# Kernel optimization log

Measured on AMD Instinct MI355X. Metric: run time of the kernel, lower is better.

The kernel has to match this reference:

```python
import jax, jax.numpy as jnp
import numpy as np

B, S, D, F = 8, 2048, 1024, 3072
EPS = 1e-6


def _rmsnorm(x, w):
    rms = jax.lax.rsqrt(jnp.mean(x * x, axis=-1, keepdims=True) + EPS)
    return x * rms * w


def _scan_causal(x_scan, a):
    # h_t = a_t * h_{t-1} + x_t, over time axis. x_scan, a: [B,S,D]
    def step(h, inp):
        xs, at = inp
        h = at * h + xs
        return h, h
    xs_t = jnp.swapaxes(x_scan, 0, 1)  # [S,B,D]
    a_t = jnp.swapaxes(a, 0, 1)
    h0 = jnp.zeros(x_scan.shape[::2], dtype=x_scan.dtype)  # [B,D]
    _, out = jax.lax.scan(step, h0, (xs_t, a_t))
    return jnp.swapaxes(out, 0, 1)  # [B,S,D]


def setup_inputs() -> dict:
    key = jax.random.key(0)
    ks = jax.random.split(key, 12)
    sd = 1.0 / np.sqrt(D)
    sf = 1.0 / np.sqrt(F)
    return {
        "x": jax.random.normal(ks[0], (B, S, D), dtype=jnp.float32),
        "rms_mix_w": jnp.ones((D,), jnp.float32),
        "rms_ffn_w": jnp.ones((D,), jnp.float32),
        "Wg": jax.random.uniform(ks[1], (D, D), jnp.float32, -sd, sd),
        "bg": jax.random.uniform(ks[2], (D,), jnp.float32, -sd, sd),
        "Wv": jax.random.uniform(ks[3], (D, D), jnp.float32, -sd, sd),
        "bv": jax.random.uniform(ks[4], (D,), jnp.float32, -sd, sd),
        "Wd": jax.random.uniform(ks[5], (D, D), jnp.float32, -sd, sd),
        "bd": jnp.full((D,), 1.0, jnp.float32),  # decay_bias_init = 1.0
        "W_gate": jax.random.uniform(ks[6], (F, D), jnp.float32, -sd, sd),
        "W_up": jax.random.uniform(ks[7], (F, D), jnp.float32, -sd, sd),
        "W_out": jax.random.uniform(ks[8], (D, F), jnp.float32, -sf, sf),
    }


def reference(x, rms_mix_w, rms_ffn_w, Wg, bg, Wv, bv, Wd, bd, W_gate, W_up, W_out):
    # --- MinGRU mixer with pre-RMSNorm and residual ---
    xn = _rmsnorm(x, rms_mix_w)
    g = jnp.einsum("bsd,ed->bse", xn, Wg) + bg
    v = jnp.einsum("bsd,ed->bse", xn, Wv) + bv
    d = jnp.einsum("bsd,ed->bse", xn, Wd) + bd
    x_scan = jax.nn.sigmoid(g) * jnp.tanh(v)
    a = 0.001 + 0.998 * jax.nn.sigmoid(d)
    x = x + _scan_causal(x_scan, a)
    # --- SwiGLU FFN with pre-RMSNorm and residual ---
    xn = _rmsnorm(x, rms_ffn_w)
    gate = jax.nn.silu(jnp.einsum("bsd,fd->bsf", xn, W_gate))
    up = jnp.einsum("bsd,fd->bsf", xn, W_up)
    x = x + jnp.einsum("bsf,df->bsd", gate * up, W_out)
    return x
```

## Files before the change

### kernel.cpp

```cpp
#include <hip/hip_runtime.h>
#include <cstdint>
#include <cstddef>

typedef unsigned short u16;
typedef __attribute__((ext_vector_type(4))) float f32x4;
typedef __attribute__((ext_vector_type(8))) short s16x8;

#define BB 8
#define SS 2048
#define DD 1024
#define FF 3072
#define MM (BB*SS)
#define NCH 64
#define LCH (SS/NCH)

__device__ __forceinline__ float bf2f(u16 u){ union{uint32_t i;float f;}v; v.i=((uint32_t)u)<<16; return v.f; }
__device__ __forceinline__ u16 f2bf(float f){ union{float f;uint32_t i;}v; v.f=f; uint32_t r=v.i+0x7FFFu+((v.i>>16)&1u); return (u16)(r>>16); }
__device__ __forceinline__ float sigm(float x){ return 1.f/(1.f+__expf(-x)); }
__device__ __forceinline__ float tanh_f(float x){ return 2.f*sigm(2.f*x)-1.f; }

__global__ void conv_gvd(const float* __restrict__ Wg, const float* __restrict__ Wv,
                         const float* __restrict__ Wd, u16* __restrict__ out){
  size_t i = ((size_t)blockIdx.x*256 + threadIdx.x)*4;
  int row = (int)(i >> 10); int col = (int)(i & 1023);
  const float* src; int srow;
  if (row < 2048) { int grp = row >> 5, w = row & 31; src = (w < 16) ? Wg : Wv; srow = grp*16 + (w & 15); }
  else            { src = Wd; srow = row - 2048; }
  float4 v = *(const float4*)(src + (size_t)srow*1024 + col);
  ushort4 o; o.x=f2bf(v.x); o.y=f2bf(v.y); o.z=f2bf(v.z); o.w=f2bf(v.w);
  *(ushort4*)(out + i) = o;
}

__global__ void conv_gu(const float* __restrict__ Wgate, const float* __restrict__ Wup,
                        u16* __restrict__ out){
  size_t i = ((size_t)blockIdx.x*256 + threadIdx.x)*4;
  int row = (int)(i >> 10); int col = (int)(i & 1023);
  int group = row >> 5, w = row & 31;
  const float* src = (w < 16) ? Wgate : Wup;
  int srow = group*16 + (w & 15);
  float4 v = *(const float4*)(src + (size_t)srow*1024 + col);
  ushort4 o; o.x=f2bf(v.x); o.y=f2bf(v.y); o.z=f2bf(v.z); o.w=f2bf(v.w);
  *(ushort4*)(out + i) = o;
}

__global__ void conv_cp(const float* __restrict__ W, u16* __restrict__ out){
  size_t i = ((size_t)blockIdx.x*256 + threadIdx.x)*4;
  float4 v = *(const float4*)(W + i);
  ushort4 o; o.x=f2bf(v.x); o.y=f2bf(v.y); o.z=f2bf(v.z); o.w=f2bf(v.w);
  *(ushort4*)(out + i) = o;
}

__global__ void rmsnorm_k(const float* __restrict__ x, const float* __restrict__ wgt,
                          u16* __restrict__ out){
  const int row = blockIdx.x, t = threadIdx.x;
  float4 v = ((const float4*)(x + (size_t)row*DD))[t];
  float ss = v.x*v.x + v.y*v.y + v.z*v.z + v.w*v.w;
  #pragma unroll
  for (int o = 32; o > 0; o >>= 1) ss += __shfl_down(ss, o, 64);
  __shared__ float sacc[4];
  if ((t & 63) == 0) sacc[t >> 6] = ss;
  __syncthreads();
  float tot = sacc[0] + sacc[1] + sacc[2] + sacc[3];
  float r = rsqrtf(tot * (1.f/(float)DD) + 1e-6f);
  float4 wv = ((const float4*)wgt)[t];
  ushort4 o; o.x=f2bf(v.x*r*wv.x); o.y=f2bf(v.y*r*wv.y); o.z=f2bf(v.z*r*wv.z); o.w=f2bf(v.w*r*wv.w);
  ((ushort4*)(out + (size_t)row*DD))[t] = o;
}

template<int EPI, int NTN>
__global__ __launch_bounds__(512) void gemm256(
    const u16* __restrict__ A, const u16* __restrict__ Bm, int K,
    const float* __restrict__ bg, const float* __restrict__ bv, const float* __restrict__ bd,
    u16* __restrict__ o_xs, u16* __restrict__ o_a,
    u16* __restrict__ o_h, float* __restrict__ o_y)
{
  __shared__ u16 lds[2*32768];
  const int tid = threadIdx.x, w = tid >> 6, l = tid & 63;
  const int wr = w >> 2, wc = w & 3;
  const int nwg = gridDim.x, bid = blockIdx.x;
  const int sw = (bid & 7) * (nwg >> 3) + (bid >> 3);
  const int tm = sw / NTN, tn = sw % NTN;

  const int srow  = w*8 + (l >> 3);
  const int sslot = (l & 7) ^ ((l >> 3) & 7);
  const u16* gA = A  + (size_t)(tm*256 + srow)*K + sslot*8;
  const u16* gB = Bm + (size_t)(tn*256 + srow)*K + sslot*8;

#define STAGE_HALF(dbuf, isB, h, tile) do { \
    const u16* gsrc_ = ((isB) ? gB : gA) + ((size_t)(h)*128)*K + (size_t)(tile)*64; \
    u16* ldst_ = &lds[(dbuf)*32768 + (isB)*16384 + (h)*8192 + w*512]; \
    __builtin_amdgcn_global_load_lds((const __attribute__((address_space(1))) void*)gsrc_, \
        (__attribute__((address_space(3))) void*)ldst_, 16, 0, 0); \
    __builtin_amdgcn_global_load_lds((const __attribute__((address_space(1))) void*)(gsrc_ + (size_t)64*K), \
        (__attribute__((address_space(3))) void*)(ldst_ + 4096), 16, 0, 0); \
  } while(0)

  const int aRow = wr*128 + (l & 15);
  const int bRow = wc*64  + (l & 15);
  const int sl0  = (((l >> 4) ^ (l & 7))) * 8;

#define LDA(cb, mi, ks) (*(const s16x8*)&lds[(cb)*32768 + (aRow + (mi)*16)*64 + (sl0 ^ ((ks)*32))])
#define LDB(cb, ni, ks) (*(const s16x8*)&lds[(cb)*32768 + 16384 + (bRow + (ni)*16)*64 + (sl0 ^ ((ks)*32))])

#define LOADB(cb) do { \
    bfr[0][0]=LDB(cb,0,0); bfr[0][1]=LDB(cb,0,1); \
    bfr[1][0]=LDB(cb,1,0); bfr[1][1]=LDB(cb,1,1); \
    bfr[2][0]=LDB(cb,2,0); bfr[2][1]=LDB(cb,2,1); \
    bfr[3][0]=LDB(cb,3,0); bfr[3][1]=LDB(cb,3,1); \
  } while(0)

#define PHASE(cb, mi0, STAGE_STMT, ...) do { \
    s16x8 a00 = LDA(cb, (mi0),   0), a01 = LDA(cb, (mi0),   1); \
    s16x8 a10 = LDA(cb, (mi0)+1, 0), a11 = LDA(cb, (mi0)+1, 1); \
    STAGE_STMT; \
    __builtin_amdgcn_s_barrier(); \
    asm volatile("s_waitcnt lgkmcnt(0)" ::: "memory"); \
    __builtin_amdgcn_s_setprio(1); \
    acc[(mi0)  ][0] = __builtin_amdgcn_mfma_f32_16x16x32_bf16(a00, bfr[0][0], acc[(mi0)  ][0],0,0,0); \
    acc[(mi0)  ][1] = __builtin_amdgcn_mfma_f32_16x16x32_bf16(a00, bfr[1][0], acc[(mi0)  ][1],0,0,0); \
    acc[(mi0)  ][2] = __builtin_amdgcn_mfma_f32_16x16x32_bf16(a00, bfr[2][0], acc[(mi0)  ][2],0,0,0); \
    acc[(mi0)  ][3] = __builtin_amdgcn_mfma_f32_16x16x32_bf16(a00, bfr[3][0], acc[(mi0)  ][3],0,0,0); \
    acc[(mi0)+1][0] = __builtin_amdgcn_mfma_f32_16x16x32_bf16(a10, bfr[0][0], acc[(mi0)+1][0],0,0,0); \
    acc[(mi0)+1][1] = __builtin_amdgcn_mfma_f32_16x16x32_bf16(a10, bfr[1][0], acc[(mi0)+1][1],0,0,0); \
    acc[(mi0)+1][2] = __builtin_amdgcn_mfma_f32_16x16x32_bf16(a10, bfr[2][0], acc[(mi0)+1][2],0,0,0); \
    acc[(mi0)+1][3] = __builtin_amdgcn_mfma_f32_16x16x32_bf16(a10, bfr[3][0], acc[(mi0)+1][3],0,0,0); \
    acc[(mi0)  ][0] = __builtin_amdgcn_mfma_f32_16x16x32_bf16(a01, bfr[0][1], acc[(mi0)  ][0],0,0,0); \
    acc[(mi0)  ][1] = __builtin_amdgcn_mfma_f32_16x16x32_bf16(a01, bfr[1][1], acc[(mi0)  ][1],0,0,0); \
    acc[(mi0)  ][2] = __builtin_amdgcn_mfma_f32_16x16x32_bf16(a01, bfr[2][1], acc[(mi0)  ][2],0,0,0); \
    acc[(mi0)  ][3] = __builtin_amdgcn_mfma_f32_16x16x32_bf16(a01, bfr[3][1], acc[(mi0)  ][3],0,0,0); \
    acc[(mi0)+1][0] = __builtin_amdgcn_mfma_f32_16x16x32_bf16(a11, bfr[0][1], acc[(mi0)+1][0],0,0,0); \
    acc[(mi0)+1][1] = __builtin_amdgcn_mfma_f32_16x16x32_bf16(a11, bfr[1][1], acc[(mi0)+1][1],0,0,0); \
    acc[(mi0)+1][2] = __builtin_amdgcn_mfma_f32_16x16x32_bf16(a11, bfr[2][1], acc[(mi0)+1][2],0,0,0); \
    acc[(mi0)+1][3] = __builtin_amdgcn_mfma_f32_16x16x32_bf16(a11, bfr[3][1], acc[(mi0)+1][3],0,0,0); \
    __builtin_amdgcn_s_setprio(0); \
    __VA_ARGS__; \
    __builtin_amdgcn_s_barrier(); \
  } while(0)

  f32x4 acc[8][4] = {};
  s16x8 bfr[4][2];
  const int nk = K >> 6;

  STAGE_HALF(0,0,0,0); STAGE_HALF(0,0,1,0);
  STAGE_HALF(0,1,0,0); STAGE_HALF(0,1,1,0);
  STAGE_HALF(1,1,0,1); STAGE_HALF(1,1,1,1);
  asm volatile("s_waitcnt vmcnt(4)" ::: "memory");
  __builtin_amdgcn_s_barrier();

  for (int it = 0, t = 0; it < (nk >> 1); ++it, t += 2) {
    const int tp1 = t + 1;
    int tp2 = t + 2; if (tp2 >= nk) tp2 -= nk;
    int tp3 = t + 3; if (tp3 >= nk) tp3 -= nk;
    LOADB(0);
    PHASE(0, 0, STAGE_HALF(1,0,0,tp1), );
    PHASE(0, 2, STAGE_HALF(1,0,1,tp1), );
    PHASE(0, 4, STAGE_HALF(0,1,0,tp2), );
    PHASE(0, 6, STAGE_HALF(0,1,1,tp2), asm volatile("s_waitcnt vmcnt(4)" ::: "memory"));
    LOADB(1);
    PHASE(1, 0, STAGE_HALF(0,0,0,tp2), );
    PHASE(1, 2, STAGE_HALF(0,0,1,tp2), );
    PHASE(1, 4, STAGE_HALF(1,1,0,tp3), );
    PHASE(1, 6, STAGE_HALF(1,1,1,tp3), asm volatile("s_waitcnt vmcnt(4)" ::: "memory"));
  }
#undef PHASE
#undef LOADB
#undef LDA
#undef LDB
#undef STAGE_HALF

  const int rb = tm*256 + wr*128 + ((l >> 4) << 2);
  const int lc = l & 15;
  if constexpr (EPI == 0) {
    if (tn < 8) {
      #pragma unroll
      for (int mi = 0; mi < 8; ++mi)
        #pragma unroll
        for (int j = 0; j < 2; ++j) {
          int f = tn*128 + wc*32 + j*16 + lc;
          float bgf = bg[f], bvf = bv[f];
          #pragma unroll
          for (int i = 0; i < 4; ++i) {
            int r = rb + mi*16 + i;
            float g2 = acc[mi][2*j][i]   + bgf;
            float v2 = acc[mi][2*j+1][i] + bvf;
            o_xs[(size_t)r*DD + f] = f2bf(sigm(g2) * tanh_f(v2));
          }
        }
    } else {
      #pragma unroll
      for (int mi = 0; mi < 8; ++mi)
        #pragma unroll
        for (int ni = 0; ni < 4; ++ni) {
          int c = (tn-8)*256 + wc*64 + ni*16 + lc;
          float bdc = bd[c];
          #pragma unroll
          for (int i = 0; i < 4; ++i) {
            int r = rb + mi*16 + i;
            o_a[(size_t)r*DD + c] = f2bf(0.001f + 0.998f*sigm(acc[mi][ni][i] + bdc));
          }
        }
    }
  } else if constexpr (EPI == 1) {
    #pragma unroll
    for (int mi = 0; mi < 8; ++mi)
      #pragma unroll
      for (int j = 0; j < 2; ++j) {
        int f = tn*128 + wc*32 + j*16 + lc;
        #pragma unroll
        for (int i = 0; i < 4; ++i) {
          int r = rb + mi*16 + i;
          float g2 = acc[mi][2*j][i], u2 = acc[mi][2*j+1][i];
          o_h[(size_t)r*FF + f] = f2bf(g2 * sigm(g2) * u2);
        }
      }
  } else {
    #pragma unroll
    for (int mi = 0; mi < 8; ++mi)
      #pragma unroll
      for (int ni = 0; ni < 4; ++ni) {
        int c = tn*256 + wc*64 + ni*16 + lc;
        #pragma unroll
        for (int i = 0; i < 4; ++i) {
          int r = rb + mi*16 + i;
          size_t idx = (size_t)r*DD + c;
          o_y[idx] = o_y[idx] + acc[mi][ni][i];
        }
      }
  }
}

__global__ void scan_pass1(const u16* __restrict__ xs, const u16* __restrict__ ab,
                           float* __restrict__ Ac, float* __restrict__ Xc){
  const int bid = blockIdx.x;
  const int d = ((bid & 3) << 8) + threadIdx.x;
  const int c = (bid >> 2) & (NCH-1);
  const int b = bid >> 8;
  size_t base = ((size_t)b*SS + (size_t)c*LCH)*DD + d;
  float A = 1.f, X = 0.f;
  for (int tt = 0; tt < LCH; ++tt){
    size_t idx = base + (size_t)tt*DD;
    float a = bf2f(ab[idx]);
    X = a*X + bf2f(xs[idx]); A *= a;
  }
  size_t o = ((size_t)b*NCH + c)*DD + d;
  Ac[o] = A; Xc[o] = X;
}

__global__ void scan_pass2(const float* __restrict__ Ac, const float* __restrict__ Xc,
                           float* __restrict__ hin){
  int gid = blockIdx.x*256 + threadIdx.x;
  int b = gid >> 10, d = gid & 1023;
  float h = 0.f;
  for (int c = 0; c < NCH; ++c){
    size_t o = ((size_t)b*NCH + c)*DD + d;
    hin[o] = h;
    h = Ac[o]*h + Xc[o];
  }
}

__global__ __launch_bounds__(256) void scan_pass3_norm(
    const u16* __restrict__ xs, const u16* __restrict__ ab,
    const float* __restrict__ hin, const float* __restrict__ x,
    const float* __restrict__ rfw, float* __restrict__ y, u16* __restrict__ xn)
{
  const int bid = blockIdx.x;
  const int c = bid & (NCH-1);
  const int b = bid >> 6;
  const int t = threadIdx.x;
  float h[4], w[4];
  size_t hb = ((size_t)b*NCH + c)*DD + t;
  #pragma unroll
  for (int j = 0; j < 4; ++j){ h[j] = hin[hb + j*256]; w[j] = rfw[t + j*256]; }
  __shared__ float sred[4];
  size_t base = ((size_t)b*SS + (size_t)c*LCH)*DD + t;
  for (int tt = 0; tt < LCH; ++tt){
    size_t rowb = base + (size_t)tt*DD;
    float yv[4]; float ss = 0.f;
    #pragma unroll
    for (int j = 0; j < 4; ++j){
      size_t idx = rowb + (size_t)j*256;
      float a = bf2f(ab[idx]);
      h[j] = a*h[j] + bf2f(xs[idx]);
      yv[j] = x[idx] + h[j];
      y[idx] = yv[j];
      ss += yv[j]*yv[j];
    }
    #pragma unroll
    for (int o = 32; o > 0; o >>= 1) ss += __shfl_down(ss, o, 64);
    if ((t & 63) == 0) sred[t >> 6] = ss;
    __syncthreads();
    float tot = sred[0] + sred[1] + sred[2] + sred[3];
    float r = rsqrtf(tot * (1.f/(float)DD) + 1e-6f);
    #pragma unroll
    for (int j = 0; j < 4; ++j){
      size_t idx = rowb + (size_t)j*256;
      xn[idx] = f2bf(yv[j]*r*w[j]);
    }
    __syncthreads();
  }
}

extern "C" void kernel_launch(void* const* d_in, const int* in_sizes, int n_in,
                              void* d_out, int out_size, void* d_ws, size_t ws_size,
                              hipStream_t stream) {
  const float* x     = (const float*)d_in[0];
  const float* rmw   = (const float*)d_in[1];
  const float* rfw   = (const float*)d_in[2];
  const float* Wg    = (const float*)d_in[3];
  const float* bg    = (const float*)d_in[4];
  const float* Wv    = (const float*)d_in[5];
  const float* bv    = (const float*)d_in[6];
  const float* Wd    = (const float*)d_in[7];
  const float* bd    = (const float*)d_in[8];
  const float* Wgate = (const float*)d_in[9];
  const float* Wup   = (const float*)d_in[10];
  const float* Wout  = (const float*)d_in[11];
  float* out = (float*)d_out;

  char* p = (char*)d_ws;
  u16*  xn    = (u16*)p;              p += (size_t)MM*DD*2;
  u16*  Wgvd  = (u16*)p;              p += (size_t)3072*1024*2;
  u16*  Wgu   = (u16*)p;              p += (size_t)6144*1024*2;
  u16*  Wo    = (u16*)p;              p += (size_t)1024*3072*2;
  char* big   = p;                    p += (size_t)MM*FF*2;
  u16*  xs    = (u16*)big;
  u16*  ab    = (u16*)(big + (size_t)MM*DD*2);
  u16*  hbuf  = (u16*)big;
  float* Ac   = (float*)p;            p += (size_t)BB*NCH*DD*4;
  float* Xc   = (float*)p;            p += (size_t)BB*NCH*DD*4;
  float* hin  = (float*)p;            p += (size_t)BB*NCH*DD*4;

  conv_gvd<<<3072, 256, 0, stream>>>(Wg, Wv, Wd, Wgvd);
  conv_gu <<<6144, 256, 0, stream>>>(Wgate, Wup, Wgu);
  conv_cp <<<3072, 256, 0, stream>>>(Wout, Wo);

  rmsnorm_k<<<MM, 256, 0, stream>>>(x, rmw, xn);
  gemm256<0,12><<<64*12, 512, 0, stream>>>(xn, Wgvd, 1024,
      bg, bv, bd, xs, ab, nullptr, nullptr);
  scan_pass1<<<BB*NCH*4, 256, 0, stream>>>(xs, ab, Ac, Xc);
  scan_pass2<<<32, 256, 0, stream>>>(Ac, Xc, hin);
  scan_pass3_norm<<<BB*NCH, 256, 0, stream>>>(xs, ab, hin, x, rfw, out, xn);

  gemm256<1,24><<<64*24, 512, 0, stream>>>(xn, Wgu, 1024,
      nullptr, nullptr, nullptr, nullptr, nullptr, hbuf, nullptr);
  gemm256<2,4><<<64*4, 512, 0, stream>>>(hbuf, Wo, 3072,
      nullptr, nullptr, nullptr, nullptr, nullptr, nullptr, out);
}
```

Measured before the change: 532.3 us.

## Fold FFN RMSNorm into GEMM epilogue, store residual in bf16, merge weight converts

The FFN RMSNorm weight is folded into the bf16 Wgate/Wup conversion, and the per-row inverse RMS is applied inside the gate/up GEMM epilogue. The scan pass therefore writes a single bf16 copy of the residual y plus a per-row scale, instead of fp32 y and a normalized bf16 xn. The output GEMM reads the bf16 residual and writes out directly, with no fp32 read-modify-write. The three weight-conversion kernels become one launch. This cuts global memory traffic and a launch, but storing the residual in bf16 costs precision in the final output.

```diff
diff --git a/kernel.cpp b/kernel.cpp
--- a/kernel.cpp
+++ b/kernel.cpp
@@ -19,35 +19,37 @@
 __device__ __forceinline__ float sigm(float x){ return 1.f/(1.f+__expf(-x)); }
 __device__ __forceinline__ float tanh_f(float x){ return 2.f*sigm(2.f*x)-1.f; }
 
-__global__ void conv_gvd(const float* __restrict__ Wg, const float* __restrict__ Wv,
-                         const float* __restrict__ Wd, u16* __restrict__ out){
-  size_t i = ((size_t)blockIdx.x*256 + threadIdx.x)*4;
-  int row = (int)(i >> 10); int col = (int)(i & 1023);
-  const float* src; int srow;
-  if (row < 2048) { int grp = row >> 5, w = row & 31; src = (w < 16) ? Wg : Wv; srow = grp*16 + (w & 15); }
-  else            { src = Wd; srow = row - 2048; }
-  float4 v = *(const float4*)(src + (size_t)srow*1024 + col);
-  ushort4 o; o.x=f2bf(v.x); o.y=f2bf(v.y); o.z=f2bf(v.z); o.w=f2bf(v.w);
-  *(ushort4*)(out + i) = o;
-}
-
-__global__ void conv_gu(const float* __restrict__ Wgate, const float* __restrict__ Wup,
-                        u16* __restrict__ out){
-  size_t i = ((size_t)blockIdx.x*256 + threadIdx.x)*4;
-  int row = (int)(i >> 10); int col = (int)(i & 1023);
-  int group = row >> 5, w = row & 31;
-  const float* src = (w < 16) ? Wgate : Wup;
-  int srow = group*16 + (w & 15);
-  float4 v = *(const float4*)(src + (size_t)srow*1024 + col);
-  ushort4 o; o.x=f2bf(v.x); o.y=f2bf(v.y); o.z=f2bf(v.z); o.w=f2bf(v.w);
-  *(ushort4*)(out + i) = o;
-}
-
-__global__ void conv_cp(const float* __restrict__ W, u16* __restrict__ out){
-  size_t i = ((size_t)blockIdx.x*256 + threadIdx.x)*4;
-  float4 v = *(const float4*)(W + i);
-  ushort4 o; o.x=f2bf(v.x); o.y=f2bf(v.y); o.z=f2bf(v.z); o.w=f2bf(v.w);
-  *(ushort4*)(out + i) = o;
+__global__ void conv_all(const float* __restrict__ Wg, const float* __restrict__ Wv,
+                         const float* __restrict__ Wd, const float* __restrict__ Wgate,
+                         const float* __restrict__ Wup, const float* __restrict__ Wout,
+                         const float* __restrict__ rfw,
+                         u16* __restrict__ oGvd, u16* __restrict__ oGu, u16* __restrict__ oWo){
+  const int blk = blockIdx.x;
+  if (blk < 3072) {
+    size_t i = ((size_t)blk*256 + threadIdx.x)*4;
+    int row = (int)(i >> 10); int col = (int)(i & 1023);
+    const float* src; int srow;
+    if (row < 2048) { int grp = row >> 5, w = row & 31; src = (w < 16) ? Wg : Wv; srow = grp*16 + (w & 15); }
+    else            { src = Wd; srow = row - 2048; }
+    float4 v = *(const float4*)(src + (size_t)srow*1024 + col);
+    ushort4 o; o.x=f2bf(v.x); o.y=f2bf(v.y); o.z=f2bf(v.z); o.w=f2bf(v.w);
+    *(ushort4*)(oGvd + i) = o;
+  } else if (blk < 9216) {
+    size_t i = ((size_t)(blk-3072)*256 + threadIdx.x)*4;
+    int row = (int)(i >> 10); int col = (int)(i & 1023);
+    int group = row >> 5, w = row & 31;
+    const float* src = (w < 16) ? Wgate : Wup;
+    int srow = group*16 + (w & 15);
+    float4 v = *(const float4*)(src + (size_t)srow*1024 + col);
+    float4 s = *(const float4*)(rfw + col);
+    ushort4 o; o.x=f2bf(v.x*s.x); o.y=f2bf(v.y*s.y); o.z=f2bf(v.z*s.z); o.w=f2bf(v.w*s.w);
+    *(ushort4*)(oGu + i) = o;
+  } else {
+    size_t i = ((size_t)(blk-9216)*256 + threadIdx.x)*4;
+    float4 v = *(const float4*)(Wout + i);
+    ushort4 o; o.x=f2bf(v.x); o.y=f2bf(v.y); o.z=f2bf(v.z); o.w=f2bf(v.w);
+    *(ushort4*)(oWo + i) = o;
+  }
 }
 
 __global__ void rmsnorm_k(const float* __restrict__ x, const float* __restrict__ wgt,
@@ -71,8 +73,9 @@
 __global__ __launch_bounds__(512) void gemm256(
     const u16* __restrict__ A, const u16* __restrict__ Bm, int K,
     const float* __restrict__ bg, const float* __restrict__ bv, const float* __restrict__ bd,
+    const float* __restrict__ rinv,
     u16* __restrict__ o_xs, u16* __restrict__ o_a,
-    u16* __restrict__ o_h, float* __restrict__ o_y)
+    u16* __restrict__ o_h, const u16* __restrict__ yres, float* __restrict__ o_out)
 {
   __shared__ u16 lds[2*32768];
   const int tid = threadIdx.x, w = tid >> 6, l = tid & 63;
@@ -202,17 +205,20 @@
     }
   } else if constexpr (EPI == 1) {
     #pragma unroll
-    for (int mi = 0; mi < 8; ++mi)
+    for (int mi = 0; mi < 8; ++mi) {
+      float4 rv = *(const float4*)&rinv[rb + mi*16];
       #pragma unroll
       for (int j = 0; j < 2; ++j) {
         int f = tn*128 + wc*32 + j*16 + lc;
         #pragma unroll
         for (int i = 0; i < 4; ++i) {
           int r = rb + mi*16 + i;
-          float g2 = acc[mi][2*j][i], u2 = acc[mi][2*j+1][i];
+          float rvi = (i==0) ? rv.x : (i==1) ? rv.y : (i==2) ? rv.z : rv.w;
+          float g2 = acc[mi][2*j][i]*rvi, u2 = acc[mi][2*j+1][i]*rvi;
           o_h[(size_t)r*FF + f] = f2bf(g2 * sigm(g2) * u2);
         }
       }
+    }
   } else {
     #pragma unroll
     for (int mi = 0; mi < 8; ++mi)
@@ -223,7 +229,7 @@
         for (int i = 0; i < 4; ++i) {
           int r = rb + mi*16 + i;
           size_t idx = (size_t)r*DD + c;
-          o_y[idx] = o_y[idx] + acc[mi][ni][i];
+          o_out[idx] = bf2f(yres[idx]) + acc[mi][ni][i];
         }
       }
   }
@@ -258,21 +264,22 @@
   }
 }
 
-__global__ __launch_bounds__(256) void scan_pass3_norm(
+__global__ __launch_bounds__(256) void scan_pass3_y(
     const u16* __restrict__ xs, const u16* __restrict__ ab,
     const float* __restrict__ hin, const float* __restrict__ x,
-    const float* __restrict__ rfw, float* __restrict__ y, u16* __restrict__ xn)
+    u16* __restrict__ ybf, float* __restrict__ rinv)
 {
   const int bid = blockIdx.x;
   const int c = bid & (NCH-1);
   const int b = bid >> 6;
   const int t = threadIdx.x;
-  float h[4], w[4];
+  float h[4];
   size_t hb = ((size_t)b*NCH + c)*DD + t;
   #pragma unroll
-  for (int j = 0; j < 4; ++j){ h[j] = hin[hb + j*256]; w[j] = rfw[t + j*256]; }
+  for (int j = 0; j < 4; ++j) h[j] = hin[hb + j*256];
   __shared__ float sred[4];
   size_t base = ((size_t)b*SS + (size_t)c*LCH)*DD + t;
+  const int row0 = b*SS + c*LCH;
   for (int tt = 0; tt < LCH; ++tt){
     size_t rowb = base + (size_t)tt*DD;
     float yv[4]; float ss = 0.f;
@@ -282,7 +289,6 @@
       float a = bf2f(ab[idx]);
       h[j] = a*h[j] + bf2f(xs[idx]);
       yv[j] = x[idx] + h[j];
-      y[idx] = yv[j];
       ss += yv[j]*yv[j];
     }
     #pragma unroll
@@ -291,10 +297,11 @@
     __syncthreads();
     float tot = sred[0] + sred[1] + sred[2] + sred[3];
     float r = rsqrtf(tot * (1.f/(float)DD) + 1e-6f);
+    if (t == 0) rinv[row0 + tt] = r;
     #pragma unroll
     for (int j = 0; j < 4; ++j){
       size_t idx = rowb + (size_t)j*256;
-      xn[idx] = f2bf(yv[j]*r*w[j]);
+      ybf[idx] = f2bf(yv[j]);
     }
     __syncthreads();
   }
@@ -329,20 +336,20 @@
   float* Ac   = (float*)p;            p += (size_t)BB*NCH*DD*4;
   float* Xc   = (float*)p;            p += (size_t)BB*NCH*DD*4;
   float* hin  = (float*)p;            p += (size_t)BB*NCH*DD*4;
-
-  conv_gvd<<<3072, 256, 0, stream>>>(Wg, Wv, Wd, Wgvd);
-  conv_gu <<<6144, 256, 0, stream>>>(Wgate, Wup, Wgu);
-  conv_cp <<<3072, 256, 0, stream>>>(Wout, Wo);
+  float* rinv = (float*)p;            p += (size_t)MM*4;
+  u16*  ybf   = xn;
+
+  conv_all<<<12288, 256, 0, stream>>>(Wg, Wv, Wd, Wgate, Wup, Wout, rfw, Wgvd, Wgu, Wo);
 
   rmsnorm_k<<<MM, 256, 0, stream>>>(x, rmw, xn);
   gemm256<0,12><<<64*12, 512, 0, stream>>>(xn, Wgvd, 1024,
-      bg, bv, bd, xs, ab, nullptr, nullptr);
+      bg, bv, bd, nullptr, xs, ab, nullptr, nullptr, nullptr);
   scan_pass1<<<BB*NCH*4, 256, 0, stream>>>(xs, ab, Ac, Xc);
   scan_pass2<<<32, 256, 0, stream>>>(Ac, Xc, hin);
-  scan_pass3_norm<<<BB*NCH, 256, 0, stream>>>(xs, ab, hin, x, rfw, out, xn);
-
-  gemm256<1,24><<<64*24, 512, 0, stream>>>(xn, Wgu, 1024,
-      nullptr, nullptr, nullptr, nullptr, nullptr, hbuf, nullptr);
+  scan_pass3_y<<<BB*NCH, 256, 0, stream>>>(xs, ab, hin, x, ybf, rinv);
+
+  gemm256<1,24><<<64*24, 512, 0, stream>>>(ybf, Wgu, 1024,
+      nullptr, nullptr, nullptr, rinv, nullptr, nullptr, hbuf, nullptr, nullptr);
   gemm256<2,4><<<64*4, 512, 0, stream>>>(hbuf, Wo, 3072,
-      nullptr, nullptr, nullptr, nullptr, nullptr, nullptr, out);
-}
+      nullptr, nullptr, nullptr, nullptr, nullptr, nullptr, nullptr, ybf, out);
+}
```

Result: faster. 511.4 us (-3.9%).
